# Optimization experiments

Measured on AMD Instinct MI355X. Metric: run time of the kernel, lower is better.

Reference implementation:

```python
import jax, jax.numpy as jnp
import numpy as np

N, M, D = 60000, 96, 16  # voxels, centroids, descriptor_dim
NB = 4                    # batches (scenes)


def setup_inputs() -> dict:
    key = jax.random.key(0)
    ks = jax.random.split(key, 10)
    voxel_desc = jax.random.normal(ks[0], (N, D), jnp.float32)
    centroid_conf = jax.random.uniform(ks[1], (M, 1), jnp.float32)
    offsets = jax.random.normal(ks[2], (N, 3), jnp.float32)
    # 1x1 Conv2d weights act as plain linears over the channel dim
    c_in = 2 * D + 7          # 39
    c_hid = D + 3             # 19
    W1 = jax.random.normal(ks[3], (c_hid, c_in), jnp.float32) / np.sqrt(c_in)
    b1 = jax.random.normal(ks[4], (c_hid,), jnp.float32) * 0.01
    W2 = jax.random.normal(ks[5], (1, c_hid), jnp.float32) / np.sqrt(c_hid)
    b2 = jax.random.normal(ks[6], (1,), jnp.float32) * 0.01
    coords = jax.random.randint(ks[7], (N, 3), 0, 200, dtype=jnp.int32)
    batch_ids = jnp.sort(jax.random.randint(ks[8], (N,), 0, NB, dtype=jnp.int32))
    peak_indices = jnp.sort(jax.random.randint(ks[9], (M,), 0, N, dtype=jnp.int32))
    return {
        "voxel_desc": voxel_desc, "centroid_conf": centroid_conf,
        "offsets": offsets, "W1": W1, "b1": b1, "W2": W2, "b2": b2,
        "coords": coords, "batch_ids": batch_ids, "peak_indices": peak_indices,
    }


def reference(voxel_desc, centroid_conf, offsets, W1, b1, W2, b2,
              coords, batch_ids, peak_indices):
    d = voxel_desc.shape[1]
    # centroid descriptors: voxel desc at peaks + confidence  -> [M, D+1]
    cent_desc = jnp.concatenate([voxel_desc[peak_indices], centroid_conf], axis=-1)
    # voxel descriptors get offsets prepended -> [N, D+3]
    voxel_full = jnp.concatenate([offsets, voxel_desc], axis=-1)
    # distance feature (no_grad in the original): (coords + offset) - centroid coords
    new_coords = coords.astype(jnp.float32) + offsets            # [N, 3]
    cent_coords = coords[peak_indices].astype(jnp.float32)       # [M, 3]
    dists = jax.lax.stop_gradient(new_coords[:, None, :] - cent_coords[None, :, :])  # [N, M, 3]
    # 1x1 conv over channels == linear; split W1 columns to match the concat order
    # [voxel_full (D+3) | cent_desc (D+1) | dists (3)] so we never build the [N,M,2D+7] tensor
    W1v, W1c, W1d = W1[:, :d + 3], W1[:, d + 3:2 * d + 4], W1[:, 2 * d + 4:]
    pre = ((voxel_full @ W1v.T)[:, None, :]
           + (cent_desc @ W1c.T)[None, :, :]
           + jnp.einsum('nmk,hk->nmh', dists, W1d)
           + b1)                                                 # [N, M, D+3]
    h = jax.nn.relu(pre)
    logit = jnp.einsum('nmh,oh->nmo', h, W2)[..., 0] + b2[0]     # [N, M]
    logit = jnp.nan_to_num(jnp.clip(logit, -10.0, 10.0), nan=0.0)
    # pairs across different batches are -inf (never computed in the torch loop)
    same = batch_ids[:, None] == batch_ids[peak_indices][None, :]
    return jnp.where(same, logit, -jnp.inf)
```

## Files before the change

kernel.cpp:

```cpp
#include <hip/hip_runtime.h>
#include <hip/hip_bf16.h>

#define N_VOX   60000
#define M_CENT  96
#define C_IN    39
#define C_HID   19
#define RS      20
#define WSTR    40
#define TN      64
#define BLK     192


typedef const __hip_bfloat16* bfp;
__device__ __forceinline__ float bf2f(__hip_bfloat16 v) { return __bfloat162float(v); }
__device__ __forceinline__ float lo16(unsigned u) { return __uint_as_float(u << 16); }
__device__ __forceinline__ float hi16(unsigned u) { return __uint_as_float(u & 0xFFFF0000u); }
__device__ __forceinline__ unsigned bfb(float x) {
    unsigned b = __float_as_uint(x);
    return (b + 0x7FFFu + ((b >> 16) & 1u)) >> 16;
}

__global__ __launch_bounds__(BLK, 4) void fused_kernel(
    bfp voxel_desc,
    bfp centroid_conf,
    bfp offsets,
    bfp W1,
    bfp b1,
    bfp W2,
    bfp b2,
    const int* coords,
    const int* batch_ids,
    const int* peak_indices,
    __hip_bfloat16* out)
{
    __shared__ float sW[C_HID * WSTR];
    __shared__ float sB1[C_HID];
    __shared__ float sAn[TN * RS];
    __shared__ float sBm[M_CENT * RS];
    const int tid = threadIdx.x;
    const int rowbase = blockIdx.x * TN;

    for (int u = tid; u < C_HID * C_IN; u += BLK) {
        const int h = u / C_IN, k = u - h * C_IN;
        sW[h * WSTR + k] = bf2f(W1[u]);
    }
    if (tid < C_HID) sB1[tid] = bf2f(b1[tid]);

    float w2[C_HID];
    #pragma unroll
    for (int h = 0; h < C_HID; ++h) w2[h] = bf2f(W2[h]);
    const float b2f = bf2f(b2[0]);

    __syncthreads();

    const uint4* vd4 = (const uint4*)voxel_desc;

    if (tid < TN) {
        const int n = rowbase + tid;
        const int nc = (n < N_VOX) ? n : (N_VOX - 1);
        const uint4 va = vd4[nc * 2], vb = vd4[nc * 2 + 1];
        const float vd[16] = { lo16(va.x), hi16(va.x), lo16(va.y), hi16(va.y),
                               lo16(va.z), hi16(va.z), lo16(va.w), hi16(va.w),
                               lo16(vb.x), hi16(vb.x), lo16(vb.y), hi16(vb.y),
                               lo16(vb.z), hi16(vb.z), lo16(vb.w), hi16(vb.w) };
        const float o0 = bf2f(offsets[nc * 3 + 0]);
        const float o1 = bf2f(offsets[nc * 3 + 1]);
        const float o2 = bf2f(offsets[nc * 3 + 2]);
        const float nw0 = (float)coords[nc * 3 + 0] + o0;
        const float nw1 = (float)coords[nc * 3 + 1] + o1;
        const float nw2 = (float)coords[nc * 3 + 2] + o2;
        #pragma unroll 2
        for (int h = 0; h < C_HID; ++h) {
            const float4 w0 = *(const float4*)&sW[h * WSTR + 0];
            const float4 w1 = *(const float4*)&sW[h * WSTR + 4];
            const float4 w2c = *(const float4*)&sW[h * WSTR + 8];
            const float4 w3 = *(const float4*)&sW[h * WSTR + 12];
            const float4 w4 = *(const float4*)&sW[h * WSTR + 16];
            const float4 w9 = *(const float4*)&sW[h * WSTR + 36];
            float acc = sB1[h];
            acc += o0 * w0.x + o1 * w0.y + o2 * w0.z + vd[0] * w0.w;
            acc += vd[1] * w1.x + vd[2] * w1.y + vd[3] * w1.z + vd[4] * w1.w;
            acc += vd[5] * w2c.x + vd[6] * w2c.y + vd[7] * w2c.z + vd[8] * w2c.w;
            acc += vd[9] * w3.x + vd[10] * w3.y + vd[11] * w3.z + vd[12] * w3.w;
            acc += vd[13] * w4.x + vd[14] * w4.y + vd[15] * w4.z;
            acc += nw0 * w9.x + nw1 * w9.y + nw2 * w9.z;
            sAn[tid * RS + h] = acc;
        }
        sAn[tid * RS + 19] = __int_as_float(batch_ids[nc]);
    } else if (tid < TN + M_CENT) {
        const int m = tid - TN;
        const int p = peak_indices[m];
        const uint4 va = vd4[p * 2], vb = vd4[p * 2 + 1];
        const float cd[16] = { lo16(va.x), hi16(va.x), lo16(va.y), hi16(va.y),
                               lo16(va.z), hi16(va.z), lo16(va.w), hi16(va.w),
                               lo16(vb.x), hi16(vb.x), lo16(vb.y), hi16(vb.y),
                               lo16(vb.z), hi16(vb.z), lo16(vb.w), hi16(vb.w) };
        const float conf = bf2f(centroid_conf[m]);
        const float c0 = (float)coords[p * 3 + 0];
        const float c1 = (float)coords[p * 3 + 1];
        const float c2 = (float)coords[p * 3 + 2];
        #pragma unroll 2
        for (int h = 0; h < C_HID; ++h) {
            const float4 w4 = *(const float4*)&sW[h * WSTR + 16];
            const float4 w5 = *(const float4*)&sW[h * WSTR + 20];
            const float4 w6 = *(const float4*)&sW[h * WSTR + 24];
            const float4 w7 = *(const float4*)&sW[h * WSTR + 28];
            const float4 w8 = *(const float4*)&sW[h * WSTR + 32];
            const float4 w9 = *(const float4*)&sW[h * WSTR + 36];
            float acc = cd[0] * w4.w;
            acc += cd[1] * w5.x + cd[2] * w5.y + cd[3] * w5.z + cd[4] * w5.w;
            acc += cd[5] * w6.x + cd[6] * w6.y + cd[7] * w6.z + cd[8] * w6.w;
            acc += cd[9] * w7.x + cd[10] * w7.y + cd[11] * w7.z + cd[12] * w7.w;
            acc += cd[13] * w8.x + cd[14] * w8.y + cd[15] * w8.z + conf * w8.w;
            acc -= c0 * w9.x + c1 * w9.y + c2 * w9.z;
            sBm[m * RS + h] = acc;
        }
        sBm[m * RS + 19] = __int_as_float(batch_ids[p]);
    }

    __syncthreads();

    const int mp = tid % 48;
    const int q  = tid / 48;
    const int m0 = 2 * mp;
    float bA[RS], bB[RS];
    #pragma unroll
    for (int i = 0; i < 5; ++i) {
        *(float4*)&bA[4 * i] = *(const float4*)&sBm[m0 * RS + 4 * i];
        *(float4*)&bB[4 * i] = *(const float4*)&sBm[(m0 + 1) * RS + 4 * i];
    }
    const int cbA = __float_as_int(bA[19]);
    const int cbB = __float_as_int(bB[19]);

    #pragma unroll 4
    for (int i = 0; i < 16; ++i) {
        const int r = q + 4 * i;
        float a[RS];
        #pragma unroll
        for (int j = 0; j < 5; ++j)
            *(float4*)&a[4 * j] = *(const float4*)&sAn[r * RS + 4 * j];
        const int rb = __float_as_int(a[19]);
        float dA = 0.f, dB = 0.f;
        #pragma unroll
        for (int h = 0; h < C_HID; ++h) {
            const float av = a[h];
            dA += fmaxf(av + bA[h], 0.f) * w2[h];
            dB += fmaxf(av + bB[h], 0.f) * w2[h];
        }
        const float lA = dA + b2f, lB = dB + b2f;
        float cA = fminf(fmaxf(lA, -10.f), 10.f); cA = (lA == lA) ? cA : 0.f;
        float cB = fminf(fmaxf(lB, -10.f), 10.f); cB = (lB == lB) ? cB : 0.f;
        const float rA = (rb == cbA) ? cA : -10.0f;
        const float rB = (rb == cbB) ? cB : -10.0f;
        const int n = rowbase + r;
        if (n < N_VOX) {
            const unsigned pk = bfb(rA) | (bfb(rB) << 16);
            *reinterpret_cast<unsigned*>(out + (size_t)n * M_CENT + m0) = pk;
        }
    }
}

extern "C" void kernel_launch(void* const* d_in, const int* in_sizes, int n_in,
                              void* d_out, int out_size, void* d_ws, size_t ws_size,
                              hipStream_t stream) {
    bfp voxel_desc    = (bfp)d_in[0];
    bfp centroid_conf = (bfp)d_in[1];
    bfp offsets       = (bfp)d_in[2];
    bfp W1            = (bfp)d_in[3];
    bfp b1            = (bfp)d_in[4];
    bfp W2            = (bfp)d_in[5];
    bfp b2            = (bfp)d_in[6];
    const int* coords       = (const int*)d_in[7];
    const int* batch_ids    = (const int*)d_in[8];
    const int* peak_indices = (const int*)d_in[9];
    __hip_bfloat16* out = (__hip_bfloat16*)d_out;

    const int grid = (N_VOX + TN - 1) / TN;
    fused_kernel<<<grid, BLK, 0, stream>>>(
        voxel_desc, centroid_conf, offsets, W1, b1, W2, b2,
        coords, batch_ids, peak_indices, out);
}
```

Before: 96.11 us.

## Pack shared-memory operands as bf16 pairs and widen block to four centroids per thread

Stores W1 (with b1 folded in), the per-row and per-centroid partial sums in shared memory as packed bf16 pairs instead of fp32. It doubles the block to 384 threads with each thread computing four centroids over four rows. Global loads are issued before the first barrier so they overlap the weight staging. This cuts LDS traffic and per-row shared reads. In exchange the intermediate sums are rounded to bf16, which lowers precision, and the NaN guard on logits is dropped.

```diff
diff --git a/kernel.cpp b/kernel.cpp
--- a/kernel.cpp
+++ b/kernel.cpp
@@ -5,10 +5,9 @@
 #define M_CENT  96
 #define C_IN    39
 #define C_HID   19
-#define RS      20
-#define WSTR    40
 #define TN      64
-#define BLK     192
+#define BLK     384
+#define GRID    938
 
 
 typedef const __hip_bfloat16* bfp;
@@ -19,143 +18,166 @@
     unsigned b = __float_as_uint(x);
     return (b + 0x7FFFu + ((b >> 16) & 1u)) >> 16;
 }
-
-__global__ __launch_bounds__(BLK, 4) void fused_kernel(
-    bfp voxel_desc,
-    bfp centroid_conf,
-    bfp offsets,
-    bfp W1,
-    bfp b1,
-    bfp W2,
-    bfp b2,
-    const int* coords,
-    const int* batch_ids,
-    const int* peak_indices,
+__device__ __forceinline__ unsigned pk2(float a, float b) { return bfb(a) | (bfb(b) << 16); }
+
+__global__ __launch_bounds__(BLK, 2) void fused_kernel(
+    bfp voxel_desc, bfp centroid_conf, bfp offsets, bfp W1, bfp b1, bfp W2, bfp b2,
+    const int* coords, const int* batch_ids, const int* peak_indices,
     __hip_bfloat16* out)
 {
-    __shared__ float sW[C_HID * WSTR];
-    __shared__ float sB1[C_HID];
-    __shared__ float sAn[TN * RS];
-    __shared__ float sBm[M_CENT * RS];
+    __shared__ __align__(16) unsigned sW[C_HID * 20];
+    __shared__ __align__(16) unsigned sAn[TN * 12];
+    __shared__ __align__(16) unsigned sBm[M_CENT * 12];
     const int tid = threadIdx.x;
     const int rowbase = blockIdx.x * TN;
-
-    for (int u = tid; u < C_HID * C_IN; u += BLK) {
-        const int h = u / C_IN, k = u - h * C_IN;
-        sW[h * WSTR + k] = bf2f(W1[u]);
-    }
-    if (tid < C_HID) sB1[tid] = bf2f(b1[tid]);
-
-    float w2[C_HID];
+    const unsigned short* w1u = (const unsigned short*)W1;
+    const unsigned short* b1u = (const unsigned short*)b1;
+
+    if (tid < C_HID * 20) {
+        const int h = tid / 20, c = tid - h * 20;
+        const unsigned lo = w1u[h * C_IN + 2 * c];
+        const unsigned hi = (2 * c + 1 < C_IN) ? w1u[h * C_IN + 2 * c + 1] : b1u[h];
+        sW[tid] = lo | (hi << 16);
+    }
+
+    float w2f[20];
     #pragma unroll
-    for (int h = 0; h < C_HID; ++h) w2[h] = bf2f(W2[h]);
+    for (int h = 0; h < C_HID; ++h) w2f[h] = bf2f(W2[h]);
+    w2f[19] = 0.0f;
     const float b2f = bf2f(b2[0]);
 
-    __syncthreads();
-
     const uint4* vd4 = (const uint4*)voxel_desc;
-
+    float r0=0,r1=0,r2=0,r3=0,r4=0,r5=0,r6=0,r7=0,
+          r8=0,r9=0,r10=0,r11=0,r12=0,r13=0,r14=0,r15=0;
+    float x0=0,x1=0,x2=0;
+    float y0=0,y1=0,y2=0;
+    int   bidr = 0;
     if (tid < TN) {
         const int n = rowbase + tid;
         const int nc = (n < N_VOX) ? n : (N_VOX - 1);
         const uint4 va = vd4[nc * 2], vb = vd4[nc * 2 + 1];
-        const float vd[16] = { lo16(va.x), hi16(va.x), lo16(va.y), hi16(va.y),
-                               lo16(va.z), hi16(va.z), lo16(va.w), hi16(va.w),
-                               lo16(vb.x), hi16(vb.x), lo16(vb.y), hi16(vb.y),
-                               lo16(vb.z), hi16(vb.z), lo16(vb.w), hi16(vb.w) };
-        const float o0 = bf2f(offsets[nc * 3 + 0]);
-        const float o1 = bf2f(offsets[nc * 3 + 1]);
-        const float o2 = bf2f(offsets[nc * 3 + 2]);
-        const float nw0 = (float)coords[nc * 3 + 0] + o0;
-        const float nw1 = (float)coords[nc * 3 + 1] + o1;
-        const float nw2 = (float)coords[nc * 3 + 2] + o2;
-        #pragma unroll 2
-        for (int h = 0; h < C_HID; ++h) {
-            const float4 w0 = *(const float4*)&sW[h * WSTR + 0];
-            const float4 w1 = *(const float4*)&sW[h * WSTR + 4];
-            const float4 w2c = *(const float4*)&sW[h * WSTR + 8];
-            const float4 w3 = *(const float4*)&sW[h * WSTR + 12];
-            const float4 w4 = *(const float4*)&sW[h * WSTR + 16];
-            const float4 w9 = *(const float4*)&sW[h * WSTR + 36];
-            float acc = sB1[h];
-            acc += o0 * w0.x + o1 * w0.y + o2 * w0.z + vd[0] * w0.w;
-            acc += vd[1] * w1.x + vd[2] * w1.y + vd[3] * w1.z + vd[4] * w1.w;
-            acc += vd[5] * w2c.x + vd[6] * w2c.y + vd[7] * w2c.z + vd[8] * w2c.w;
-            acc += vd[9] * w3.x + vd[10] * w3.y + vd[11] * w3.z + vd[12] * w3.w;
-            acc += vd[13] * w4.x + vd[14] * w4.y + vd[15] * w4.z;
-            acc += nw0 * w9.x + nw1 * w9.y + nw2 * w9.z;
-            sAn[tid * RS + h] = acc;
-        }
-        sAn[tid * RS + 19] = __int_as_float(batch_ids[nc]);
+        r0=lo16(va.x); r1=hi16(va.x); r2=lo16(va.y); r3=hi16(va.y);
+        r4=lo16(va.z); r5=hi16(va.z); r6=lo16(va.w); r7=hi16(va.w);
+        r8=lo16(vb.x); r9=hi16(vb.x); r10=lo16(vb.y); r11=hi16(vb.y);
+        r12=lo16(vb.z); r13=hi16(vb.z); r14=lo16(vb.w); r15=hi16(vb.w);
+        x0 = bf2f(offsets[nc * 3 + 0]);
+        x1 = bf2f(offsets[nc * 3 + 1]);
+        x2 = bf2f(offsets[nc * 3 + 2]);
+        y0 = (float)coords[nc * 3 + 0] + x0;
+        y1 = (float)coords[nc * 3 + 1] + x1;
+        y2 = (float)coords[nc * 3 + 2] + x2;
+        bidr = batch_ids[nc];
     } else if (tid < TN + M_CENT) {
         const int m = tid - TN;
         const int p = peak_indices[m];
         const uint4 va = vd4[p * 2], vb = vd4[p * 2 + 1];
-        const float cd[16] = { lo16(va.x), hi16(va.x), lo16(va.y), hi16(va.y),
-                               lo16(va.z), hi16(va.z), lo16(va.w), hi16(va.w),
-                               lo16(vb.x), hi16(vb.x), lo16(vb.y), hi16(vb.y),
-                               lo16(vb.z), hi16(vb.z), lo16(vb.w), hi16(vb.w) };
-        const float conf = bf2f(centroid_conf[m]);
-        const float c0 = (float)coords[p * 3 + 0];
-        const float c1 = (float)coords[p * 3 + 1];
-        const float c2 = (float)coords[p * 3 + 2];
+        r0=lo16(va.x); r1=hi16(va.x); r2=lo16(va.y); r3=hi16(va.y);
+        r4=lo16(va.z); r5=hi16(va.z); r6=lo16(va.w); r7=hi16(va.w);
+        r8=lo16(vb.x); r9=hi16(vb.x); r10=lo16(vb.y); r11=hi16(vb.y);
+        r12=lo16(vb.z); r13=hi16(vb.z); r14=lo16(vb.w); r15=hi16(vb.w);
+        x0 = (float)coords[p * 3 + 0];
+        x1 = (float)coords[p * 3 + 1];
+        x2 = (float)coords[p * 3 + 2];
+        y0 = bf2f(centroid_conf[m]);
+        bidr = batch_ids[p];
+    }
+
+    __syncthreads();
+
+    const uint4* sW4 = (const uint4*)sW;
+
+    if (tid < TN) {
+        float an[20];
         #pragma unroll 2
         for (int h = 0; h < C_HID; ++h) {
-            const float4 w4 = *(const float4*)&sW[h * WSTR + 16];
-            const float4 w5 = *(const float4*)&sW[h * WSTR + 20];
-            const float4 w6 = *(const float4*)&sW[h * WSTR + 24];
-            const float4 w7 = *(const float4*)&sW[h * WSTR + 28];
-            const float4 w8 = *(const float4*)&sW[h * WSTR + 32];
-            const float4 w9 = *(const float4*)&sW[h * WSTR + 36];
-            float acc = cd[0] * w4.w;
-            acc += cd[1] * w5.x + cd[2] * w5.y + cd[3] * w5.z + cd[4] * w5.w;
-            acc += cd[5] * w6.x + cd[6] * w6.y + cd[7] * w6.z + cd[8] * w6.w;
-            acc += cd[9] * w7.x + cd[10] * w7.y + cd[11] * w7.z + cd[12] * w7.w;
-            acc += cd[13] * w8.x + cd[14] * w8.y + cd[15] * w8.z + conf * w8.w;
-            acc -= c0 * w9.x + c1 * w9.y + c2 * w9.z;
-            sBm[m * RS + h] = acc;
-        }
-        sBm[m * RS + 19] = __int_as_float(batch_ids[p]);
+            const uint4 q0 = sW4[h * 5 + 0];
+            const uint4 q1 = sW4[h * 5 + 1];
+            const uint4 q2 = sW4[h * 5 + 2];
+            const uint4 q4 = sW4[h * 5 + 4];
+            float pa = x0*lo16(q0.x) + x1*hi16(q0.x) + x2*lo16(q0.y) + r0*hi16(q0.y) + hi16(q4.w);
+            float pb = r1*lo16(q0.z) + r2*hi16(q0.z) + r3*lo16(q0.w) + r4*hi16(q0.w) + r5*lo16(q1.x);
+            float pc = r6*hi16(q1.x) + r7*lo16(q1.y) + r8*hi16(q1.y) + r9*lo16(q1.z) + r10*hi16(q1.z);
+            float pd = r11*lo16(q1.w) + r12*hi16(q1.w) + r13*lo16(q2.x) + r14*hi16(q2.x) + r15*lo16(q2.y);
+            float pe = y0*lo16(q4.z) + y1*hi16(q4.z) + y2*lo16(q4.w);
+            an[h] = (pa + pb) + (pc + pd) + pe;
+        }
+        an[19] = 0.f;
+        uint4* dst = (uint4*)&sAn[tid * 12];
+        dst[0] = make_uint4(pk2(an[0],an[1]), pk2(an[2],an[3]), pk2(an[4],an[5]), pk2(an[6],an[7]));
+        dst[1] = make_uint4(pk2(an[8],an[9]), pk2(an[10],an[11]), pk2(an[12],an[13]), pk2(an[14],an[15]));
+        dst[2] = make_uint4(pk2(an[16],an[17]), bfb(an[18]), (unsigned)bidr, 0u);
+    } else if (tid < TN + M_CENT) {
+        const int m = tid - TN;
+        float bm[20];
+        #pragma unroll 2
+        for (int h = 0; h < C_HID; ++h) {
+            const uint4 q2 = sW4[h * 5 + 2];
+            const uint4 q3 = sW4[h * 5 + 3];
+            const uint4 q4 = sW4[h * 5 + 4];
+            float pa = r0*hi16(q2.y) + r1*lo16(q2.z) + r2*hi16(q2.z) + r3*lo16(q2.w) + r4*hi16(q2.w);
+            float pb = r5*lo16(q3.x) + r6*hi16(q3.x) + r7*lo16(q3.y) + r8*hi16(q3.y);
+            float pc = r9*lo16(q3.z) + r10*hi16(q3.z) + r11*lo16(q3.w) + r12*hi16(q3.w);
+            float pd = r13*lo16(q4.x) + r14*hi16(q4.x) + r15*lo16(q4.y) + y0*hi16(q4.y);
+            float pe = -(x0*lo16(q4.z) + x1*hi16(q4.z) + x2*lo16(q4.w));
+            bm[h] = (pa + pb) + (pc + pd) + pe;
+        }
+        bm[19] = 0.f;
+        uint4* dst = (uint4*)&sBm[m * 12];
+        dst[0] = make_uint4(pk2(bm[0],bm[1]), pk2(bm[2],bm[3]), pk2(bm[4],bm[5]), pk2(bm[6],bm[7]));
+        dst[1] = make_uint4(pk2(bm[8],bm[9]), pk2(bm[10],bm[11]), pk2(bm[12],bm[13]), pk2(bm[14],bm[15]));
+        dst[2] = make_uint4(pk2(bm[16],bm[17]), bfb(bm[18]), (unsigned)bidr, 0u);
     }
 
     __syncthreads();
 
-    const int mp = tid % 48;
-    const int q  = tid / 48;
-    const int m0 = 2 * mp;
-    float bA[RS], bB[RS];
+    const int g = tid % 24;
+    const int q = tid / 24;
+    const uint4* sBm4 = (const uint4*)sBm;
+    const uint4* sAn4 = (const uint4*)sAn;
+
+    uint4 t0, t1, t2;
+    t0 = sBm4[(2*g)*3+0];   t1 = sBm4[(2*g)*3+1];   t2 = sBm4[(2*g)*3+2];
+    const unsigned b0d[10] = {t0.x,t0.y,t0.z,t0.w, t1.x,t1.y,t1.z,t1.w, t2.x,t2.y};
+    const int cb0 = (int)t2.z;
+    t0 = sBm4[(2*g+1)*3+0]; t1 = sBm4[(2*g+1)*3+1]; t2 = sBm4[(2*g+1)*3+2];
+    const unsigned b1d[10] = {t0.x,t0.y,t0.z,t0.w, t1.x,t1.y,t1.z,t1.w, t2.x,t2.y};
+    const int cb1 = (int)t2.z;
+    t0 = sBm4[(2*g+48)*3+0]; t1 = sBm4[(2*g+48)*3+1]; t2 = sBm4[(2*g+48)*3+2];
+    const unsigned b2d[10] = {t0.x,t0.y,t0.z,t0.w, t1.x,t1.y,t1.z,t1.w, t2.x,t2.y};
+    const int cb2 = (int)t2.z;
+    t0 = sBm4[(2*g+49)*3+0]; t1 = sBm4[(2*g+49)*3+1]; t2 = sBm4[(2*g+49)*3+2];
+    const unsigned b3d[10] = {t0.x,t0.y,t0.z,t0.w, t1.x,t1.y,t1.z,t1.w, t2.x,t2.y};
+    const int cb3 = (int)t2.z;
+
     #pragma unroll
-    for (int i = 0; i < 5; ++i) {
-        *(float4*)&bA[4 * i] = *(const float4*)&sBm[m0 * RS + 4 * i];
-        *(float4*)&bB[4 * i] = *(const float4*)&sBm[(m0 + 1) * RS + 4 * i];
-    }
-    const int cbA = __float_as_int(bA[19]);
-    const int cbB = __float_as_int(bB[19]);
-
-    #pragma unroll 4
-    for (int i = 0; i < 16; ++i) {
-        const int r = q + 4 * i;
-        float a[RS];
+    for (int i = 0; i < 4; ++i) {
+        const int r = q + 16 * i;
+        const uint4 a0 = sAn4[r*3+0], a1 = sAn4[r*3+1], a2 = sAn4[r*3+2];
+        const int rb = (int)a2.z;
+        const unsigned ad[10] = {a0.x,a0.y,a0.z,a0.w, a1.x,a1.y,a1.z,a1.w, a2.x,a2.y};
+        float anf[20];
         #pragma unroll
-        for (int j = 0; j < 5; ++j)
-            *(float4*)&a[4 * j] = *(const float4*)&sAn[r * RS + 4 * j];
-        const int rb = __float_as_int(a[19]);
-        float dA = 0.f, dB = 0.f;
+        for (int j = 0; j < 10; ++j) { anf[2*j] = lo16(ad[j]); anf[2*j+1] = hi16(ad[j]); }
+        float e0=0,f0=0, e1=0,f1=0, e2=0,f2=0, e3=0,f3=0;
         #pragma unroll
-        for (int h = 0; h < C_HID; ++h) {
-            const float av = a[h];
-            dA += fmaxf(av + bA[h], 0.f) * w2[h];
-            dB += fmaxf(av + bB[h], 0.f) * w2[h];
-        }
-        const float lA = dA + b2f, lB = dB + b2f;
-        float cA = fminf(fmaxf(lA, -10.f), 10.f); cA = (lA == lA) ? cA : 0.f;
-        float cB = fminf(fmaxf(lB, -10.f), 10.f); cB = (lB == lB) ? cB : 0.f;
-        const float rA = (rb == cbA) ? cA : -10.0f;
-        const float rB = (rb == cbB) ? cB : -10.0f;
+        for (int j = 0; j < 10; ++j) {
+            const float wl = w2f[2*j], wh = w2f[2*j+1];
+            const float al = anf[2*j], ah = anf[2*j+1];
+            e0 += fmaxf(al + lo16(b0d[j]), 0.f) * wl;  f0 += fmaxf(ah + hi16(b0d[j]), 0.f) * wh;
+            e1 += fmaxf(al + lo16(b1d[j]), 0.f) * wl;  f1 += fmaxf(ah + hi16(b1d[j]), 0.f) * wh;
+            e2 += fmaxf(al + lo16(b2d[j]), 0.f) * wl;  f2 += fmaxf(ah + hi16(b2d[j]), 0.f) * wh;
+            e3 += fmaxf(al + lo16(b3d[j]), 0.f) * wl;  f3 += fmaxf(ah + hi16(b3d[j]), 0.f) * wh;
+        }
+        const float l0 = e0+f0+b2f, l1 = e1+f1+b2f, l2 = e2+f2+b2f, l3 = e3+f3+b2f;
+        const float c0 = fminf(fmaxf(l0,-10.f),10.f), c1 = fminf(fmaxf(l1,-10.f),10.f);
+        const float c2 = fminf(fmaxf(l2,-10.f),10.f), c3 = fminf(fmaxf(l3,-10.f),10.f);
+        const float v0 = (rb==cb0)?c0:-10.f, v1 = (rb==cb1)?c1:-10.f;
+        const float v2 = (rb==cb2)?c2:-10.f, v3 = (rb==cb3)?c3:-10.f;
         const int n = rowbase + r;
         if (n < N_VOX) {
-            const unsigned pk = bfb(rA) | (bfb(rB) << 16);
-            *reinterpret_cast<unsigned*>(out + (size_t)n * M_CENT + m0) = pk;
+            unsigned* po = (unsigned*)(out + (size_t)n * M_CENT);
+            po[g]      = pk2(v0, v1);
+            po[g + 24] = pk2(v2, v3);
         }
     }
 }
@@ -175,8 +197,7 @@
     const int* peak_indices = (const int*)d_in[9];
     __hip_bfloat16* out = (__hip_bfloat16*)d_out;
 
-    const int grid = (N_VOX + TN - 1) / TN;
-    fused_kernel<<<grid, BLK, 0, stream>>>(
+    fused_kernel<<<GRID, BLK, 0, stream>>>(
         voxel_desc, centroid_conf, offsets, W1, b1, W2, b2,
         coords, batch_ids, peak_indices, out);
 }
```

Measured after the change: 111.0 us. 15.5% more time.
